# Kernel tuning notes

Measured on AMD Instinct MI355X. Metric: run time of the kernel, lower is better.

Reference implementation:

```python
import jax, jax.numpy as jnp
import numpy as np

N_NODES = 50000
N_EDGES = 800000
IN_DIM, HID_DIM, OUT_DIM, N_HEADS = 256, 256, 64, 4
ATT_DIM = OUT_DIM * 2 + 1  # 129


def setup_inputs() -> dict:
    key = jax.random.key(0)
    ks = jax.random.split(key, 8)
    s = 0.05
    return {
        "x": jax.random.normal(ks[0], (N_NODES, IN_DIM), dtype=jnp.float32),
        "idx": jax.random.randint(ks[1], (2, N_EDGES), 0, N_NODES, dtype=jnp.int32),
        "elem": jax.random.uniform(ks[2], (N_EDGES,), dtype=jnp.float32),
        "W1": jax.random.normal(ks[3], (N_HEADS, IN_DIM, HID_DIM), dtype=jnp.float32) * s,
        "b1": jnp.zeros((N_HEADS, HID_DIM), jnp.float32),
        "W2": jax.random.normal(ks[4], (N_HEADS, HID_DIM, OUT_DIM), dtype=jnp.float32) * s,
        "b2": jnp.zeros((N_HEADS, OUT_DIM), jnp.float32),
        "A1": jax.random.normal(ks[5], (N_HEADS, ATT_DIM, ATT_DIM), dtype=jnp.float32) * s,
        "ab1": jnp.zeros((N_HEADS, ATT_DIM), jnp.float32),
        "A2": jax.random.normal(ks[6], (N_HEADS, ATT_DIM, 1), dtype=jnp.float32) * s,
        "ab2": jnp.zeros((N_HEADS, 1), jnp.float32),
    }


def reference(x, idx, elem, W1, b1, W2, b2, A1, ab1, A2, ab2):
    row, col = idx[0], idx[1]
    n = x.shape[0]

    def head(w1, bb1, w2, bb2, a1, aab1, a2, aab2):
        # 2-layer node MLP: [N, in] -> [N, out]
        feats = jnp.maximum(x @ w1 + bb1, 0.0) @ w2 + bb2
        # gather edge endpoints + edge value -> [E, 2*out+1]
        x_cat = jnp.concatenate([feats[row], feats[col], elem[:, None]], axis=1)
        # 2-layer edge attention MLP -> scalar per edge
        hid = jnp.maximum(x_cat @ a1 + aab1, 0.0)
        e1 = (hid @ a2 + aab2)[:, 0]
        e1 = jax.nn.leaky_relu(e1, negative_slope=0.2)
        w = jnp.exp(e1 - jnp.max(e1))  # global-max-stabilized exp
        # spmm: scatter weighted neighbor features into rows
        pooled = jax.ops.segment_sum(w[:, None] * feats[col], row, num_segments=n)
        row_sum = jax.ops.segment_sum(w, row, num_segments=n) + 1e-10
        return pooled / row_sum[:, None]  # [N, out]

    h = jax.vmap(head)(W1, b1, W2, b2, A1, ab1, A2, ab2)  # [H, N, out]
    return jnp.transpose(h, (1, 0, 2)).reshape(n, -1)  # concat heads -> [N, H*out]
```

## Files before the change

### kernel.cpp

```cpp
#include <hip/hip_runtime.h>
#include <hip/hip_bf16.h>

#define NNODES 50000
#define NEDGES 800000
#define IN_DIM 256
#define HID_DIM 256
#define OUT_DIM 64
#define NHEADS 4
#define ATT_DIM 129
#define PDIM 128
#define PJROWS 144
#define MAXD 64

#define XS_LD 264
#define FS_LD 72
#define PS_LD 144

#define LOG2E 1.44269504088896340736f

typedef unsigned short u16;
typedef unsigned char u8;
typedef unsigned int u32;
typedef __attribute__((ext_vector_type(8))) short bf16x8;
typedef __attribute__((ext_vector_type(4))) float f32x4;
typedef __attribute__((ext_vector_type(2))) float f32x2;
typedef __attribute__((ext_vector_type(2))) _Float16 h16x2;
typedef __fp16 hh2 __attribute__((ext_vector_type(2)));

__device__ __forceinline__ u16 f2bf(float f) {
  union { __hip_bfloat16 b; u16 u; } v;
  v.b = __float2bfloat16(f);
  return v.u;
}
__device__ __forceinline__ float bf2f(u16 b) {
  return __uint_as_float(((u32)b) << 16);
}
__device__ __forceinline__ h16x2 u2h2(u32 u) {
  union { u32 u; h16x2 h; } v; v.u = u; return v.h;
}
__device__ __forceinline__ u32 h2u(h16x2 h) {
  union { h16x2 h; u32 u; } v; v.h = h; return v.u;
}
__device__ __forceinline__ h16x2 pkrtz(float a, float b) {
  return __builtin_bit_cast(h16x2, __builtin_amdgcn_cvt_pkrtz(a, b));
}
__device__ __forceinline__ u32 cvt_pk_bf16(float a, float b) {
  u32 r;
  asm("v_cvt_pk_bf16_f32 %0, %1, %2" : "=v"(r) : "v"(a), "v"(b));
  return r;
}

__device__ __forceinline__ float dpp_sum8(float x) {
  int v;
  v = __builtin_amdgcn_update_dpp(0, __float_as_int(x), 0xB1, 0xF, 0xF, true);
  x += __int_as_float(v);
  v = __builtin_amdgcn_update_dpp(0, __float_as_int(x), 0x4E, 0xF, 0xF, true);
  x += __int_as_float(v);
  v = __builtin_amdgcn_update_dpp(0, __float_as_int(x), 0x141, 0xF, 0xF, true);
  x += __int_as_float(v);
  return x;
}

__global__ __launch_bounds__(256) void prep_kernel(
    const int* __restrict__ idx, const float* __restrict__ elem,
    const float* __restrict__ W1, const float* __restrict__ W2,
    const float* __restrict__ A1, const float* __restrict__ ab1,
    const float* __restrict__ A2, const float* __restrict__ ab2,
    u16* __restrict__ W1T, u16* __restrict__ W2T,
    u16* __restrict__ A1Tr, u16* __restrict__ A1Tc,
    uint4* __restrict__ thE, uint4* __restrict__ thA2, uint4* __restrict__ thB1,
    float4* __restrict__ th_tail, u32* __restrict__ cnt, u32* __restrict__ ce)
{
  int id = blockIdx.x * 256 + threadIdx.x;
  if (id < NEDGES) {
    int r = idx[id];
    u32 p = atomicAdd(&cnt[r], 1u);
    if (p < MAXD)
      ce[r * MAXD + p] = ((u32)f2bf(elem[id]) << 16) | (u32)idx[NEDGES + id];
  }
  if (id < NHEADS * 256 * 256) {
    int h = id >> 16, j = (id >> 8) & 255, k = id & 255;
    W1T[id] = f2bf(W1[(size_t)h * 65536 + k * 256 + j]);
  }
  if (id < NHEADS * 64 * 256) {
    int h = id >> 14, d = (id >> 8) & 63, j = id & 255;
    W2T[id] = f2bf(W2[(size_t)h * 16384 + j * 64 + d]);
  }
  if (id < NHEADS * PJROWS * 64) {
    int h = id / (PJROWS * 64);
    int rem = id % (PJROWS * 64);
    int j = rem >> 6, d = rem & 63;
    A1Tr[id] = (j < ATT_DIM) ? f2bf(A1[(size_t)h * 16641 + d * ATT_DIM + j]) : (u16)0;
    A1Tc[id] = (j < ATT_DIM) ? f2bf(A1[(size_t)h * 16641 + (64 + d) * ATT_DIM + j]) : (u16)0;
  }
  if (id < NHEADS * 16) {
    int h = id >> 4, m = id & 15;
    const float* Erow = A1 + (size_t)h * 16641 + (size_t)128 * ATT_DIM;
    uint4 e, a, b;
    u32* ep = (u32*)&e; u32* ap = (u32*)&a; u32* bp = (u32*)&b;
#pragma unroll
    for (int p = 0; p < 4; ++p) {
      int j = m * 8 + 2 * p;
      ep[p] = h2u(pkrtz(Erow[j], Erow[j + 1]));
      ap[p] = h2u(pkrtz(A2[h * ATT_DIM + j] * LOG2E, A2[h * ATT_DIM + j + 1] * LOG2E));
      bp[p] = h2u(pkrtz(ab1[h * ATT_DIM + j], ab1[h * ATT_DIM + j + 1]));
    }
    thE[id] = e; thA2[id] = a; thB1[id] = b;
  }
  if (id < NHEADS) {
    const float* Erow = A1 + (size_t)id * 16641 + (size_t)128 * ATT_DIM;
    th_tail[id] = make_float4(Erow[128], ab1[id * ATT_DIM + 128],
                              A2[id * ATT_DIM + 128] * LOG2E, ab2[id] * LOG2E);
  }
}

__global__ __launch_bounds__(256) void mlp_mfma_kernel(
    const float* __restrict__ x, const u16* __restrict__ W1T,
    const float* __restrict__ b1, const u16* __restrict__ W2T,
    const float* __restrict__ b2, const u16* __restrict__ A1Tr,
    const u16* __restrict__ A1Tc, u8* __restrict__ PF,
    u8* __restrict__ Pr8, u16* __restrict__ Prt, u16* __restrict__ Pct)
{
  __shared__ u16 xs[64 * XS_LD];
  __shared__ u16 hs[64 * XS_LD];
  __shared__ u16 fs[64 * FS_LD];
  u8* pc_s = (u8*)hs;
  u8* pr_s = (u8*)hs + 64 * PS_LD;
  const int n0 = blockIdx.x * 64;
  const int t = threadIdx.x;
  const int wv = t >> 6;
  const int l = t & 63;
  const int lr = l & 15;
  const int lq = l >> 4;

#pragma unroll
  for (int q = 0; q < 16; ++q) {
    int fi = q * 256 + t;
    int row = fi >> 6, c4 = fi & 63;
    int n = n0 + row;
    float4 v = make_float4(0.f, 0.f, 0.f, 0.f);
    if (n < NNODES) v = *(const float4*)(x + (size_t)n * IN_DIM + c4 * 4);
    ushort4 o;
    o.x = f2bf(v.x); o.y = f2bf(v.y); o.z = f2bf(v.z); o.w = f2bf(v.w);
    *(ushort4*)&xs[row * XS_LD + c4 * 4] = o;
  }
  __syncthreads();

  for (int hi = 0; hi < 2; ++hi) {
    const int h = (int)blockIdx.y + hi * 2;

    f32x4 acc[4][4];
#pragma unroll
    for (int ji = 0; ji < 4; ++ji)
#pragma unroll
      for (int ni = 0; ni < 4; ++ni) acc[ji][ni] = f32x4{0.f, 0.f, 0.f, 0.f};

    const u16* W1b = W1T + ((size_t)h * 256 + wv * 64) * 256;
#pragma unroll
    for (int kk = 0; kk < 8; ++kk) {
      const int ko = kk * 32 + lq * 8;
      bf16x8 w[4], xv[4];
#pragma unroll
      for (int ji = 0; ji < 4; ++ji)
        w[ji] = *(const bf16x8*)(W1b + (size_t)(ji * 16 + lr) * 256 + ko);
#pragma unroll
      for (int ni = 0; ni < 4; ++ni)
        xv[ni] = *(const bf16x8*)&xs[(ni * 16 + lr) * XS_LD + ko];
#pragma unroll
      for (int ji = 0; ji < 4; ++ji)
#pragma unroll
        for (int ni = 0; ni < 4; ++ni)
          acc[ji][ni] = __builtin_amdgcn_mfma_f32_16x16x32_bf16(w[ji], xv[ni], acc[ji][ni], 0, 0, 0);
    }
#pragma unroll
    for (int ji = 0; ji < 4; ++ji) {
      float4 bv = *(const float4*)(b1 + h * HID_DIM + wv * 64 + ji * 16 + lq * 4);
#pragma unroll
      for (int ni = 0; ni < 4; ++ni) {
        f32x4 v = acc[ji][ni];
        u32 lo = cvt_pk_bf16(fmaxf(v[0] + bv.x, 0.f), fmaxf(v[1] + bv.y, 0.f));
        u32 hi2 = cvt_pk_bf16(fmaxf(v[2] + bv.z, 0.f), fmaxf(v[3] + bv.w, 0.f));
        *(uint2*)&hs[(ni * 16 + lr) * XS_LD + wv * 64 + ji * 16 + lq * 4] = make_uint2(lo, hi2);
      }
    }
    __syncthreads();

    f32x4 acc2[4];
#pragma unroll
    for (int ni = 0; ni < 4; ++ni) acc2[ni] = f32x4{0.f, 0.f, 0.f, 0.f};
    const u16* W2b = W2T + ((size_t)h * 64 + wv * 16) * 256;
#pragma unroll
    for (int kk = 0; kk < 8; ++kk) {
      const int ko = kk * 32 + lq * 8;
      bf16x8 wd = *(const bf16x8*)(W2b + (size_t)lr * 256 + ko);
#pragma unroll
      for (int ni = 0; ni < 4; ++ni) {
        bf16x8 hv = *(const bf16x8*)&hs[(ni * 16 + lr) * XS_LD + ko];
        acc2[ni] = __builtin_amdgcn_mfma_f32_16x16x32_bf16(wd, hv, acc2[ni], 0, 0, 0);
      }
    }
    __syncthreads();
    {
      float4 bv = *(const float4*)(b2 + h * OUT_DIM + wv * 16 + lq * 4);
      const int d0 = wv * 16 + lq * 4;
#pragma unroll
      for (int ni = 0; ni < 4; ++ni) {
        f32x4 v = acc2[ni];
        u32 lo = cvt_pk_bf16(v[0] + bv.x, v[1] + bv.y);
        u32 hi2 = cvt_pk_bf16(v[2] + bv.z, v[3] + bv.w);
        *(uint2*)&fs[(ni * 16 + lr) * FS_LD + d0] = make_uint2(lo, hi2);
      }
    }
    __syncthreads();

    for (int c = wv; c < 18; c += 4) {
      const int rc = c / 9;
      const int nf = c % 9;
      const u16* Ab = (rc ? A1Tc : A1Tr) + ((size_t)h * PJROWS + nf * 16) * 64;
      f32x4 acc3[4];
#pragma unroll
      for (int ni = 0; ni < 4; ++ni) acc3[ni] = f32x4{0.f, 0.f, 0.f, 0.f};
#pragma unroll
      for (int kk = 0; kk < 2; ++kk) {
        const int ko = kk * 32 + lq * 8;
        bf16x8 aj = *(const bf16x8*)(Ab + (size_t)lr * 64 + ko);
#pragma unroll
        for (int ni = 0; ni < 4; ++ni) {
          bf16x8 fv = *(const bf16x8*)&fs[(ni * 16 + lr) * FS_LD + ko];
          acc3[ni] = __builtin_amdgcn_mfma_f32_16x16x32_bf16(aj, fv, acc3[ni], 0, 0, 0);
        }
      }
#pragma unroll
      for (int ni = 0; ni < 4; ++ni) {
        const int node = ni * 16 + lr;
        int n = n0 + node;
        if (n >= NNODES) continue;
        if (nf == 8) {
          if (lq == 0) {
            u16 vb = f2bf(acc3[ni][0]);
            if (rc == 0) Prt[(size_t)h * NNODES + n] = vb;
            else         Pct[(size_t)n * NHEADS + h] = vb;
          }
        } else {
          const int j0 = nf * 16 + lq * 4;
          f32x4 v = acc3[ni];
          u32 pk = __builtin_amdgcn_cvt_pk_fp8_f32(v[0], v[1], 0, false);
          pk = __builtin_amdgcn_cvt_pk_fp8_f32(v[2], v[3], pk, true);
          if (rc == 0) *(u32*)(pr_s + node * PS_LD + j0) = pk;
          else         *(u32*)(pc_s + node * PS_LD + j0) = pk;
        }
      }
    }
    __syncthreads();

#pragma unroll
    for (int it = 0; it < 4; ++it) {
      int flat = it * 256 + t;
      int node = flat >> 4, sub = flat & 15;
      int n = n0 + node;
      if (n < NNODES) {
        uint4 v;
        if (sub < 8) v = *(const uint4*)(pc_s + node * PS_LD + sub * 16);
        else         v = *(const uint4*)((const u8*)&fs[node * FS_LD] + (sub - 8) * 16);
        *(uint4*)(PF + (size_t)n * 1024 + h * 256 + sub * 16) = v;
      }
    }
#pragma unroll
    for (int it = 0; it < 2; ++it) {
      int flat = it * 256 + t;
      int node = flat >> 3, sub = flat & 7;
      int n = n0 + node;
      if (n < NNODES) {
        uint4 v = *(const uint4*)(pr_s + node * PS_LD + sub * 16);
        *(uint4*)(Pr8 + ((size_t)h * NNODES + n) * PDIM + sub * 16) = v;
      }
    }
    __syncthreads();
  }
}

__global__ __launch_bounds__(256) void edge_csr_kernel(
    const u8* __restrict__ PF, const u8* __restrict__ Pr8,
    const u16* __restrict__ Prt, const u16* __restrict__ Pct,
    const u32* __restrict__ cnt, const u32* __restrict__ ce,
    const uint4* __restrict__ thE, const uint4* __restrict__ thA2,
    const uint4* __restrict__ thB1, const float4* __restrict__ th_tail,
    float* __restrict__ out)
{
  const int r = blockIdx.x;
  const int h = threadIdx.x >> 6;
  const int l = threadIdx.x & 63;
  const int g = l >> 3;
  const int m = l & 7;

  const int deg = min((int)cnt[r], MAXD);
  if (deg == 0) {
    if (g == 0) {
      float4 z = make_float4(0.f, 0.f, 0.f, 0.f);
      float* o = out + (size_t)r * (NHEADS * OUT_DIM) + h * OUT_DIM + m * 8;
      *(float4*)o = z; *(float4*)(o + 4) = z;
    }
    return;
  }

  h16x2 Ej2[8], a2v2[8], prb2[8];
  {
    uint4 pr8v = *(const uint4*)(Pr8 + ((size_t)h * NNODES + r) * PDIM + m * 16);
    const u32* pw = (const u32*)&pr8v;
#pragma unroll
    for (int half = 0; half < 2; ++half) {
      uint4 Eu = thE[h * 16 + 2 * m + half];
      uint4 Au = thA2[h * 16 + 2 * m + half];
      uint4 Bu = thB1[h * 16 + 2 * m + half];
      const u32* ep = (const u32*)&Eu;
      const u32* ap = (const u32*)&Au;
      const u32* bp = (const u32*)&Bu;
#pragma unroll
      for (int p = 0; p < 2; ++p) {
        u32 w8 = pw[half * 2 + p];
        f32x2 qa = __builtin_amdgcn_cvt_pk_f32_fp8((int)w8, false);
        f32x2 qb = __builtin_amdgcn_cvt_pk_f32_fp8((int)w8, true);
        int o = half * 4 + p * 2;
        Ej2[o]      = u2h2(ep[p * 2]);
        Ej2[o + 1]  = u2h2(ep[p * 2 + 1]);
        a2v2[o]     = u2h2(ap[p * 2]);
        a2v2[o + 1] = u2h2(ap[p * 2 + 1]);
        prb2[o]     = pkrtz(qa[0], qa[1]) + u2h2(bp[p * 2]);
        prb2[o + 1] = pkrtz(qb[0], qb[1]) + u2h2(bp[p * 2 + 1]);
      }
    }
  }
  const float4 tl = th_tail[h];
  float Et = 0.f, prtb = 0.f, a2t = 0.f;
  if (m == 0) {
    Et = tl.x;
    prtb = bf2f(Prt[(size_t)h * NNODES + r]) + tl.y;
    a2t = tl.z;
  }
  const float ab2v = tl.w;
  const h16x2 zero2 = {(_Float16)0.f, (_Float16)0.f};
  const u8* PFh = PF + h * 256;

  const u32* cebase = ce + r * MAXD;

  float acc[8];
#pragma unroll
  for (int q = 0; q < 8; ++q) acc[q] = 0.f;
  float wsum = 0.f;

  for (int k0 = 0; k0 < deg; k0 += 8) {
    const int e0 = k0 + g;
    u32 cv = cebase[(e0 < deg) ? e0 : (deg - 1)];
    u32 coloff = (cv & 0xffffu) << 10;
    float el = __uint_as_float(cv & 0xffff0000u);

    uint4 pc = *(const uint4*)(PFh + coloff + m * 16);
    uint4 f4 = *(const uint4*)(PFh + coloff + 128 + m * 16);
    float pctv = (m == 0) ? bf2f(Pct[(coloff >> 8) + h]) : 0.f;

    float tsum = fmaxf(fmaf(el, Et, prtb + pctv), 0.f) * a2t;

    const u32* pcw = (const u32*)&pc;
    const h16x2 el2 = pkrtz(el, el);
#pragma unroll
    for (int p = 0; p < 4; ++p) {
      f32x2 va = __builtin_amdgcn_cvt_pk_f32_fp8((int)pcw[p], false);
      f32x2 vb = __builtin_amdgcn_cvt_pk_f32_fp8((int)pcw[p], true);
      h16x2 s0 = prb2[p * 2] + pkrtz(va[0], va[1]);
      h16x2 s1 = prb2[p * 2 + 1] + pkrtz(vb[0], vb[1]);
      s0 = __builtin_elementwise_fma(el2, Ej2[p * 2], s0);
      s1 = __builtin_elementwise_fma(el2, Ej2[p * 2 + 1], s1);
      s0 = __builtin_elementwise_max(s0, zero2);
      s1 = __builtin_elementwise_max(s1, zero2);
      tsum = __builtin_amdgcn_fdot2(__builtin_bit_cast(hh2, s0),
                                    __builtin_bit_cast(hh2, a2v2[p * 2]), tsum, false);
      tsum = __builtin_amdgcn_fdot2(__builtin_bit_cast(hh2, s1),
                                    __builtin_bit_cast(hh2, a2v2[p * 2 + 1]), tsum, false);
    }

    tsum = dpp_sum8(tsum);

    float e1f = tsum + ab2v;
    e1f = fmaxf(e1f, 0.2f * e1f);
    float w = exp2f(e1f);
    w = (e0 < deg) ? w : 0.f;

    const u32* fw = (const u32*)&f4;
#pragma unroll
    for (int p = 0; p < 4; ++p) {
      acc[p * 2]     = fmaf(w, __uint_as_float(fw[p] << 16), acc[p * 2]);
      acc[p * 2 + 1] = fmaf(w, __uint_as_float(fw[p] & 0xffff0000u), acc[p * 2 + 1]);
    }
    wsum += w;
  }

#pragma unroll
  for (int sh = 8; sh <= 32; sh <<= 1) {
#pragma unroll
    for (int q = 0; q < 8; ++q) acc[q] += __shfl_xor(acc[q], sh);
    wsum += __shfl_xor(wsum, sh);
  }
  if (g == 0) {
    float inv = 1.0f / (wsum + 1e-10f);
    float* o = out + (size_t)r * (NHEADS * OUT_DIM) + h * OUT_DIM + m * 8;
    *(float4*)o = make_float4(acc[0] * inv, acc[1] * inv, acc[2] * inv, acc[3] * inv);
    *(float4*)(o + 4) = make_float4(acc[4] * inv, acc[5] * inv, acc[6] * inv, acc[7] * inv);
  }
}

extern "C" void kernel_launch(void* const* d_in, const int* in_sizes, int n_in,
                              void* d_out, int out_size, void* d_ws, size_t ws_size,
                              hipStream_t stream) {
  const float* x    = (const float*)d_in[0];
  const int*   idx  = (const int*)d_in[1];
  const float* elem = (const float*)d_in[2];
  const float* W1   = (const float*)d_in[3];
  const float* b1   = (const float*)d_in[4];
  const float* W2   = (const float*)d_in[5];
  const float* b2   = (const float*)d_in[6];
  const float* A1   = (const float*)d_in[7];
  const float* ab1  = (const float*)d_in[8];
  const float* A2   = (const float*)d_in[9];
  const float* ab2  = (const float*)d_in[10];
  float* out = (float*)d_out;

  u8*  Pr8 = (u8*)d_ws;
  u8*  PF  = Pr8 + (size_t)NHEADS * NNODES * PDIM;
  u16* Prt = (u16*)(PF + (size_t)NNODES * 1024);
  u16* Pct = Prt + (size_t)NHEADS * NNODES;
  u32* cnt = (u32*)(Pct + (size_t)NHEADS * NNODES);
  u32* ce  = cnt + NNODES;
  u16* W1T  = (u16*)(ce + (size_t)NNODES * MAXD);
  u16* W2T  = W1T + NHEADS * 256 * 256;
  u16* A1Tr = W2T + NHEADS * 64 * 256;
  u16* A1Tc = A1Tr + NHEADS * PJROWS * 64;
  uint4* thE  = (uint4*)(A1Tc + NHEADS * PJROWS * 64);
  uint4* thA2 = thE + NHEADS * 16;
  uint4* thB1 = thA2 + NHEADS * 16;
  float4* th_tail = (float4*)(thB1 + NHEADS * 16);

  (void)hipMemsetAsync(cnt, 0, (size_t)NNODES * sizeof(u32), stream);

  prep_kernel<<<(NEDGES + 255) / 256, 256, 0, stream>>>(
      idx, elem, W1, W2, A1, ab1, A2, ab2, W1T, W2T, A1Tr, A1Tc,
      thE, thA2, thB1, th_tail, cnt, ce);

  dim3 gridM((NNODES + 63) / 64, 2);
  mlp_mfma_kernel<<<gridM, 256, 0, stream>>>(x, W1T, b1, W2T, b2, A1Tr, A1Tc,
                                             PF, Pr8, Prt, Pct);

  edge_csr_kernel<<<NNODES, 256, 0, stream>>>(PF, Pr8, Prt, Pct, cnt, ce,
                                              thE, thA2, thB1, th_tail, out);
}
```

Measured before the change: 316.6 us.

## Pre-convert x to bf16 and give each MLP block a single head

The fp32→bf16 conversion of x moves into the prep kernel, which writes it to a workspace buffer. The MLP kernel now handles one head per block (grid y = 4 instead of 2 heads per block) and loads its x fragments straight from global bf16 memory instead of staging them in shared memory. This removes the duplicate per-block conversion, lowers shared-memory use and doubles the number of blocks. The cost is an extra bf16 copy of x written and read through global memory, and reads that run past the last node row into adjacent workspace; those values are masked out later.

```diff
diff --git a/kernel.cpp b/kernel.cpp
--- a/kernel.cpp
+++ b/kernel.cpp
@@ -62,16 +62,26 @@
 }
 
 __global__ __launch_bounds__(256) void prep_kernel(
-    const int* __restrict__ idx, const float* __restrict__ elem,
-    const float* __restrict__ W1, const float* __restrict__ W2,
-    const float* __restrict__ A1, const float* __restrict__ ab1,
-    const float* __restrict__ A2, const float* __restrict__ ab2,
+    const float* __restrict__ x, const int* __restrict__ idx,
+    const float* __restrict__ elem, const float* __restrict__ W1,
+    const float* __restrict__ W2, const float* __restrict__ A1,
+    const float* __restrict__ ab1, const float* __restrict__ A2,
+    const float* __restrict__ ab2, u16* __restrict__ xb,
     u16* __restrict__ W1T, u16* __restrict__ W2T,
     u16* __restrict__ A1Tr, u16* __restrict__ A1Tc,
     uint4* __restrict__ thE, uint4* __restrict__ thA2, uint4* __restrict__ thB1,
     float4* __restrict__ th_tail, u32* __restrict__ cnt, u32* __restrict__ ce)
 {
   int id = blockIdx.x * 256 + threadIdx.x;
+  {
+    float4 a = *(const float4*)(x + (size_t)id * 8);
+    float4 b = *(const float4*)(x + (size_t)id * 8 + 4);
+    ushort4 o0, o1;
+    o0.x = f2bf(a.x); o0.y = f2bf(a.y); o0.z = f2bf(a.z); o0.w = f2bf(a.w);
+    o1.x = f2bf(b.x); o1.y = f2bf(b.y); o1.z = f2bf(b.z); o1.w = f2bf(b.w);
+    *(ushort4*)(xb + (size_t)id * 8) = o0;
+    *(ushort4*)(xb + (size_t)id * 8 + 4) = o1;
+  }
   if (id < NEDGES) {
     int r = idx[id];
     u32 p = atomicAdd(&cnt[r], 1u);
@@ -115,17 +125,17 @@
 }
 
 __global__ __launch_bounds__(256) void mlp_mfma_kernel(
-    const float* __restrict__ x, const u16* __restrict__ W1T,
+    const u16* __restrict__ xb, const u16* __restrict__ W1T,
     const float* __restrict__ b1, const u16* __restrict__ W2T,
     const float* __restrict__ b2, const u16* __restrict__ A1Tr,
     const u16* __restrict__ A1Tc, u8* __restrict__ PF,
     u8* __restrict__ Pr8, u16* __restrict__ Prt, u16* __restrict__ Pct)
 {
-  __shared__ u16 xs[64 * XS_LD];
   __shared__ u16 hs[64 * XS_LD];
   __shared__ u16 fs[64 * FS_LD];
   u8* pc_s = (u8*)hs;
   u8* pr_s = (u8*)hs + 64 * PS_LD;
+  const int h = blockIdx.y;
   const int n0 = blockIdx.x * 64;
   const int t = threadIdx.x;
   const int wv = t >> 6;
@@ -133,149 +143,132 @@
   const int lr = l & 15;
   const int lq = l >> 4;
 
-#pragma unroll
-  for (int q = 0; q < 16; ++q) {
-    int fi = q * 256 + t;
-    int row = fi >> 6, c4 = fi & 63;
-    int n = n0 + row;
-    float4 v = make_float4(0.f, 0.f, 0.f, 0.f);
-    if (n < NNODES) v = *(const float4*)(x + (size_t)n * IN_DIM + c4 * 4);
-    ushort4 o;
-    o.x = f2bf(v.x); o.y = f2bf(v.y); o.z = f2bf(v.z); o.w = f2bf(v.w);
-    *(ushort4*)&xs[row * XS_LD + c4 * 4] = o;
+  f32x4 acc[4][4];
+#pragma unroll
+  for (int ji = 0; ji < 4; ++ji)
+#pragma unroll
+    for (int ni = 0; ni < 4; ++ni) acc[ji][ni] = f32x4{0.f, 0.f, 0.f, 0.f};
+
+  const u16* W1b = W1T + ((size_t)h * 256 + wv * 64) * 256;
+  const u16* xbb = xb + (size_t)n0 * IN_DIM;
+#pragma unroll
+  for (int kk = 0; kk < 8; ++kk) {
+    const int ko = kk * 32 + lq * 8;
+    bf16x8 w[4], xv[4];
+#pragma unroll
+    for (int ji = 0; ji < 4; ++ji)
+      w[ji] = *(const bf16x8*)(W1b + (size_t)(ji * 16 + lr) * 256 + ko);
+#pragma unroll
+    for (int ni = 0; ni < 4; ++ni)
+      xv[ni] = *(const bf16x8*)(xbb + (size_t)(ni * 16 + lr) * IN_DIM + ko);
+#pragma unroll
+    for (int ji = 0; ji < 4; ++ji)
+#pragma unroll
+      for (int ni = 0; ni < 4; ++ni)
+        acc[ji][ni] = __builtin_amdgcn_mfma_f32_16x16x32_bf16(w[ji], xv[ni], acc[ji][ni], 0, 0, 0);
+  }
+#pragma unroll
+  for (int ji = 0; ji < 4; ++ji) {
+    float4 bv = *(const float4*)(b1 + h * HID_DIM + wv * 64 + ji * 16 + lq * 4);
+#pragma unroll
+    for (int ni = 0; ni < 4; ++ni) {
+      f32x4 v = acc[ji][ni];
+      u32 lo = cvt_pk_bf16(fmaxf(v[0] + bv.x, 0.f), fmaxf(v[1] + bv.y, 0.f));
+      u32 hi2 = cvt_pk_bf16(fmaxf(v[2] + bv.z, 0.f), fmaxf(v[3] + bv.w, 0.f));
+      *(uint2*)&hs[(ni * 16 + lr) * XS_LD + wv * 64 + ji * 16 + lq * 4] = make_uint2(lo, hi2);
+    }
   }
   __syncthreads();
 
-  for (int hi = 0; hi < 2; ++hi) {
-    const int h = (int)blockIdx.y + hi * 2;
-
-    f32x4 acc[4][4];
-#pragma unroll
-    for (int ji = 0; ji < 4; ++ji)
-#pragma unroll
-      for (int ni = 0; ni < 4; ++ni) acc[ji][ni] = f32x4{0.f, 0.f, 0.f, 0.f};
-
-    const u16* W1b = W1T + ((size_t)h * 256 + wv * 64) * 256;
-#pragma unroll
-    for (int kk = 0; kk < 8; ++kk) {
+  f32x4 acc2[4];
+#pragma unroll
+  for (int ni = 0; ni < 4; ++ni) acc2[ni] = f32x4{0.f, 0.f, 0.f, 0.f};
+  const u16* W2b = W2T + ((size_t)h * 64 + wv * 16) * 256;
+#pragma unroll
+  for (int kk = 0; kk < 8; ++kk) {
+    const int ko = kk * 32 + lq * 8;
+    bf16x8 wd = *(const bf16x8*)(W2b + (size_t)lr * 256 + ko);
+#pragma unroll
+    for (int ni = 0; ni < 4; ++ni) {
+      bf16x8 hv = *(const bf16x8*)&hs[(ni * 16 + lr) * XS_LD + ko];
+      acc2[ni] = __builtin_amdgcn_mfma_f32_16x16x32_bf16(wd, hv, acc2[ni], 0, 0, 0);
+    }
+  }
+  __syncthreads();
+  {
+    float4 bv = *(const float4*)(b2 + h * OUT_DIM + wv * 16 + lq * 4);
+    const int d0 = wv * 16 + lq * 4;
+#pragma unroll
+    for (int ni = 0; ni < 4; ++ni) {
+      f32x4 v = acc2[ni];
+      u32 lo = cvt_pk_bf16(v[0] + bv.x, v[1] + bv.y);
+      u32 hi2 = cvt_pk_bf16(v[2] + bv.z, v[3] + bv.w);
+      *(uint2*)&fs[(ni * 16 + lr) * FS_LD + d0] = make_uint2(lo, hi2);
+    }
+  }
+  __syncthreads();
+
+  for (int c = wv; c < 18; c += 4) {
+    const int rc = c / 9;
+    const int nf = c % 9;
+    const u16* Ab = (rc ? A1Tc : A1Tr) + ((size_t)h * PJROWS + nf * 16) * 64;
+    f32x4 acc3[4];
+#pragma unroll
+    for (int ni = 0; ni < 4; ++ni) acc3[ni] = f32x4{0.f, 0.f, 0.f, 0.f};
+#pragma unroll
+    for (int kk = 0; kk < 2; ++kk) {
       const int ko = kk * 32 + lq * 8;
-      bf16x8 w[4], xv[4];
-#pragma unroll
-      for (int ji = 0; ji < 4; ++ji)
-        w[ji] = *(const bf16x8*)(W1b + (size_t)(ji * 16 + lr) * 256 + ko);
-#pragma unroll
-      for (int ni = 0; ni < 4; ++ni)
-        xv[ni] = *(const bf16x8*)&xs[(ni * 16 + lr) * XS_LD + ko];
-#pragma unroll
-      for (int ji = 0; ji < 4; ++ji)
-#pragma unroll
-        for (int ni = 0; ni < 4; ++ni)
-          acc[ji][ni] = __builtin_amdgcn_mfma_f32_16x16x32_bf16(w[ji], xv[ni], acc[ji][ni], 0, 0, 0);
-    }
-#pragma unroll
-    for (int ji = 0; ji < 4; ++ji) {
-      float4 bv = *(const float4*)(b1 + h * HID_DIM + wv * 64 + ji * 16 + lq * 4);
+      bf16x8 aj = *(const bf16x8*)(Ab + (size_t)lr * 64 + ko);
 #pragma unroll
       for (int ni = 0; ni < 4; ++ni) {
-        f32x4 v = acc[ji][ni];
-        u32 lo = cvt_pk_bf16(fmaxf(v[0] + bv.x, 0.f), fmaxf(v[1] + bv.y, 0.f));
-        u32 hi2 = cvt_pk_bf16(fmaxf(v[2] + bv.z, 0.f), fmaxf(v[3] + bv.w, 0.f));
-        *(uint2*)&hs[(ni * 16 + lr) * XS_LD + wv * 64 + ji * 16 + lq * 4] = make_uint2(lo, hi2);
+        bf16x8 fv = *(const bf16x8*)&fs[(ni * 16 + lr) * FS_LD + ko];
+        acc3[ni] = __builtin_amdgcn_mfma_f32_16x16x32_bf16(aj, fv, acc3[ni], 0, 0, 0);
       }
     }
-    __syncthreads();
-
-    f32x4 acc2[4];
-#pragma unroll
-    for (int ni = 0; ni < 4; ++ni) acc2[ni] = f32x4{0.f, 0.f, 0.f, 0.f};
-    const u16* W2b = W2T + ((size_t)h * 64 + wv * 16) * 256;
-#pragma unroll
-    for (int kk = 0; kk < 8; ++kk) {
-      const int ko = kk * 32 + lq * 8;
-      bf16x8 wd = *(const bf16x8*)(W2b + (size_t)lr * 256 + ko);
-#pragma unroll
-      for (int ni = 0; ni < 4; ++ni) {
-        bf16x8 hv = *(const bf16x8*)&hs[(ni * 16 + lr) * XS_LD + ko];
-        acc2[ni] = __builtin_amdgcn_mfma_f32_16x16x32_bf16(wd, hv, acc2[ni], 0, 0, 0);
+#pragma unroll
+    for (int ni = 0; ni < 4; ++ni) {
+      const int node = ni * 16 + lr;
+      int n = n0 + node;
+      if (n >= NNODES) continue;
+      if (nf == 8) {
+        if (lq == 0) {
+          u16 vb = f2bf(acc3[ni][0]);
+          if (rc == 0) Prt[(size_t)h * NNODES + n] = vb;
+          else         Pct[(size_t)n * NHEADS + h] = vb;
+        }
+      } else {
+        const int j0 = nf * 16 + lq * 4;
+        f32x4 v = acc3[ni];
+        u32 pk = __builtin_amdgcn_cvt_pk_fp8_f32(v[0], v[1], 0, false);
+        pk = __builtin_amdgcn_cvt_pk_fp8_f32(v[2], v[3], pk, true);
+        if (rc == 0) *(u32*)(pr_s + node * PS_LD + j0) = pk;
+        else         *(u32*)(pc_s + node * PS_LD + j0) = pk;
       }
     }
-    __syncthreads();
-    {
-      float4 bv = *(const float4*)(b2 + h * OUT_DIM + wv * 16 + lq * 4);
-      const int d0 = wv * 16 + lq * 4;
-#pragma unroll
-      for (int ni = 0; ni < 4; ++ni) {
-        f32x4 v = acc2[ni];
-        u32 lo = cvt_pk_bf16(v[0] + bv.x, v[1] + bv.y);
-        u32 hi2 = cvt_pk_bf16(v[2] + bv.z, v[3] + bv.w);
-        *(uint2*)&fs[(ni * 16 + lr) * FS_LD + d0] = make_uint2(lo, hi2);
-      }
-    }
-    __syncthreads();
-
-    for (int c = wv; c < 18; c += 4) {
-      const int rc = c / 9;
-      const int nf = c % 9;
-      const u16* Ab = (rc ? A1Tc : A1Tr) + ((size_t)h * PJROWS + nf * 16) * 64;
-      f32x4 acc3[4];
-#pragma unroll
-      for (int ni = 0; ni < 4; ++ni) acc3[ni] = f32x4{0.f, 0.f, 0.f, 0.f};
-#pragma unroll
-      for (int kk = 0; kk < 2; ++kk) {
-        const int ko = kk * 32 + lq * 8;
-        bf16x8 aj = *(const bf16x8*)(Ab + (size_t)lr * 64 + ko);
-#pragma unroll
-        for (int ni = 0; ni < 4; ++ni) {
-          bf16x8 fv = *(const bf16x8*)&fs[(ni * 16 + lr) * FS_LD + ko];
-          acc3[ni] = __builtin_amdgcn_mfma_f32_16x16x32_bf16(aj, fv, acc3[ni], 0, 0, 0);
-        }
-      }
-#pragma unroll
-      for (int ni = 0; ni < 4; ++ni) {
-        const int node = ni * 16 + lr;
-        int n = n0 + node;
-        if (n >= NNODES) continue;
-        if (nf == 8) {
-          if (lq == 0) {
-            u16 vb = f2bf(acc3[ni][0]);
-            if (rc == 0) Prt[(size_t)h * NNODES + n] = vb;
-            else         Pct[(size_t)n * NHEADS + h] = vb;
-          }
-        } else {
-          const int j0 = nf * 16 + lq * 4;
-          f32x4 v = acc3[ni];
-          u32 pk = __builtin_amdgcn_cvt_pk_fp8_f32(v[0], v[1], 0, false);
-          pk = __builtin_amdgcn_cvt_pk_fp8_f32(v[2], v[3], pk, true);
-          if (rc == 0) *(u32*)(pr_s + node * PS_LD + j0) = pk;
-          else         *(u32*)(pc_s + node * PS_LD + j0) = pk;
-        }
-      }
-    }
-    __syncthreads();
-
-#pragma unroll
-    for (int it = 0; it < 4; ++it) {
-      int flat = it * 256 + t;
-      int node = flat >> 4, sub = flat & 15;
-      int n = n0 + node;
-      if (n < NNODES) {
-        uint4 v;
-        if (sub < 8) v = *(const uint4*)(pc_s + node * PS_LD + sub * 16);
-        else         v = *(const uint4*)((const u8*)&fs[node * FS_LD] + (sub - 8) * 16);
-        *(uint4*)(PF + (size_t)n * 1024 + h * 256 + sub * 16) = v;
-      }
-    }
-#pragma unroll
-    for (int it = 0; it < 2; ++it) {
-      int flat = it * 256 + t;
-      int node = flat >> 3, sub = flat & 7;
-      int n = n0 + node;
-      if (n < NNODES) {
-        uint4 v = *(const uint4*)(pr_s + node * PS_LD + sub * 16);
-        *(uint4*)(Pr8 + ((size_t)h * NNODES + n) * PDIM + sub * 16) = v;
-      }
-    }
-    __syncthreads();
+  }
+  __syncthreads();
+
+#pragma unroll
+  for (int it = 0; it < 4; ++it) {
+    int flat = it * 256 + t;
+    int node = flat >> 4, sub = flat & 15;
+    int n = n0 + node;
+    if (n < NNODES) {
+      uint4 v;
+      if (sub < 8) v = *(const uint4*)(pc_s + node * PS_LD + sub * 16);
+      else         v = *(const uint4*)((const u8*)&fs[node * FS_LD] + (sub - 8) * 16);
+      *(uint4*)(PF + (size_t)n * 1024 + h * 256 + sub * 16) = v;
+    }
+  }
+#pragma unroll
+  for (int it = 0; it < 2; ++it) {
+    int flat = it * 256 + t;
+    int node = flat >> 3, sub = flat & 7;
+    int n = n0 + node;
+    if (n < NNODES) {
+      uint4 v = *(const uint4*)(pr_s + node * PS_LD + sub * 16);
+      *(uint4*)(Pr8 + ((size_t)h * NNODES + n) * PDIM + sub * 16) = v;
+    }
   }
 }
 
@@ -424,7 +417,8 @@
   const float* ab2  = (const float*)d_in[10];
   float* out = (float*)d_out;
 
-  u8*  Pr8 = (u8*)d_ws;
+  u16* xb  = (u16*)d_ws;
+  u8*  Pr8 = (u8*)(xb + (size_t)NNODES * IN_DIM);
   u8*  PF  = Pr8 + (size_t)NHEADS * NNODES * PDIM;
   u16* Prt = (u16*)(PF + (size_t)NNODES * 1024);
   u16* Pct = Prt + (size_t)NHEADS * NNODES;
@@ -441,12 +435,12 @@
 
   (void)hipMemsetAsync(cnt, 0, (size_t)NNODES * sizeof(u32), stream);
 
-  prep_kernel<<<(NEDGES + 255) / 256, 256, 0, stream>>>(
-      idx, elem, W1, W2, A1, ab1, A2, ab2, W1T, W2T, A1Tr, A1Tc,
+  prep_kernel<<<NNODES * IN_DIM / 8 / 256, 256, 0, stream>>>(
+      x, idx, elem, W1, W2, A1, ab1, A2, ab2, xb, W1T, W2T, A1Tr, A1Tc,
       thE, thA2, thB1, th_tail, cnt, ce);
 
-  dim3 gridM((NNODES + 63) / 64, 2);
-  mlp_mfma_kernel<<<gridM, 256, 0, stream>>>(x, W1T, b1, W2T, b2, A1Tr, A1Tc,
+  dim3 gridM((NNODES + 63) / 64, NHEADS);
+  mlp_mfma_kernel<<<gridM, 256, 0, stream>>>(xb, W1T, b1, W2T, b2, A1Tr, A1Tc,
                                              PF, Pr8, Prt, Pct);
 
   edge_csr_kernel<<<NNODES, 256, 0, stream>>>(PF, Pr8, Prt, Pct, cnt, ce,
```

Result: slower. 327.4 us (+3.4%).
